# Kernel tuning notes

Measured on AMD Instinct MI355X. Metric: run time of the kernel, lower is better.

The kernel has to match this reference:

```python
import jax, jax.numpy as jnp
import numpy as np

# dims (see shape_source)
B, S, V, E, H, L, F = 512, 17, 40002, 1024, 16, 12, 4096
DH = E // H          # per-head dim = hidden_size // num_attention_heads
NREL = 500           # num_relations
NEDGE = 100          # num_edges (edge-label vocab)
BIG = 1000000.0


def _ln(x, g, b, eps):
    m = jnp.mean(x, axis=-1, keepdims=True)
    v = jnp.mean((x - m) ** 2, axis=-1, keepdims=True)
    return (x - m) * jax.lax.rsqrt(v + eps) * g + b


def setup_inputs() -> dict:
    key = jax.random.key(0)
    ks = jax.random.split(key, 24)
    n = lambda k, sh: 0.02 * jax.random.normal(k, sh, jnp.float32)
    inp = {
        # runtime inputs
        'input_ids': jax.random.randint(ks[0], (B, S), 0, V),
        'input_mask': jnp.ones((B, S), jnp.float32),
        'edge_labels': jax.random.randint(ks[1], (S, S), 0, NEDGE),
        'mask_pos': jax.random.randint(ks[2], (B,), 0, S),
        'mask_label': jax.random.randint(ks[3], (B,), 0, V),
        'mask_type': jnp.ones((B, 1), jnp.float32),  # +1 => entity slot masked
        'confidence': jax.random.uniform(ks[4], (B,), jnp.float32),
        # parameters
        'node_emb': n(ks[5], (V, E)),
        'edge_k': n(ks[6], (NEDGE, DH)),
        'edge_v': n(ks[7], (NEDGE, DH)),
        'ln1_g': jnp.ones((E,), jnp.float32), 'ln1_b': jnp.zeros((E,), jnp.float32),
        'Wq': n(ks[8], (L, E, E)), 'bq': jnp.zeros((L, E), jnp.float32),
        'Wk': n(ks[9], (L, E, E)), 'bk': jnp.zeros((L, E), jnp.float32),
        'Wv': n(ks[10], (L, E, E)), 'bv': jnp.zeros((L, E), jnp.float32),
        'Wo': n(ks[11], (L, E, E)), 'bo': jnp.zeros((L, E), jnp.float32),
        'lnA_g': jnp.ones((L, E), jnp.float32), 'lnA_b': jnp.zeros((L, E), jnp.float32),
        'W1': n(ks[12], (L, E, F)), 'b1': jnp.zeros((L, F), jnp.float32),
        'W2': n(ks[13], (L, F, E)), 'b2': jnp.zeros((L, E), jnp.float32),
        'lnF_g': jnp.ones((L, E), jnp.float32), 'lnF_b': jnp.zeros((L, E), jnp.float32),
        'ln2_g': jnp.ones((E,), jnp.float32), 'ln2_b': jnp.zeros((E,), jnp.float32),
        'fc2_bias': jnp.zeros((V,), jnp.float32),
    }
    return inp


def _forward(node_emb, edge_k, edge_v, ln1_g, ln1_b,
             Wq, bq, Wk, bk, Wv, bv, Wo, bo, lnA_g, lnA_b,
             W1, b1, W2, b2, lnF_g, lnF_b, ln2_g, ln2_b, fc2_bias,
             input_mask, mask_type, confidence,
             input_ids, edge_labels, mask_pos, mask_label):
    # embedding + pre-LN (dropout is identity in eval mode)
    x = _ln(node_emb[input_ids], ln1_g, ln1_b, 1e-12)          # [B,S,E]
    em = jnp.sign(edge_labels).astype(x.dtype)[:, :, None]     # [S,S,1]
    ek = edge_k[edge_labels] * em                              # [S,S,DH]
    ev = edge_v[edge_labels] * em
    m = input_mask[:, :, None]                                 # [B,S,1]
    attn_bias = (BIG * (m @ jnp.swapaxes(m, 1, 2) - 1.0))[:, None]  # [B,1,S,S]

    def step(h, p):
        wq, bq_, wk, bk_, wv, bv_, wo, bo_, ga, ba, w1, b1_, w2, b2_, gf, bf = p
        proj = lambda w, b: (h @ w + b).reshape(B, S, H, DH).transpose(0, 2, 1, 3)
        q = proj(wq, bq_) * (DH ** -0.5)
        k = proj(wk, bk_)
        v = proj(wv, bv_)
        # edge-aware attention scores: content + edge-key bias
        s = jnp.einsum('bhqd,bhkd->bhqk', q, k) \
            + jnp.einsum('bhqd,qkd->bhqk', q, ek) + attn_bias
        a = jax.nn.softmax(s, axis=-1)
        c = jnp.einsum('bhqk,bhkd->bhqd', a, v) \
            + jnp.einsum('bhqk,qkd->bhqd', a, ev)
        y = c.transpose(0, 2, 1, 3).reshape(B, S, E) @ wo + bo_
        h = _ln(h + y, ga, ba, 1e-12)                          # post-LN (cmd 'dan')
        f = jax.nn.gelu(h @ w1 + b1_, approximate=False) @ w2 + b2_
        return _ln(h + f, gf, bf, 1e-12), None

    enc, _ = jax.lax.scan(step, x, (Wq, bq, Wk, bk, Wv, bv, Wo, bo,
                                    lnA_g, lnA_b, W1, b1, W2, b2, lnF_g, lnF_b))

    # mode == 'normal': gather masked position (fc1 output is dead code in the original)
    hm = enc[jnp.arange(B), mask_pos]                          # [B,E]
    hm = _ln(jax.nn.gelu(hm, approximate=False), ln2_g, ln2_b, 1e-7)
    logits = hm @ node_emb.T + fc2_bias                        # tied projection [B,V]

    ti = jnp.concatenate([-jnp.ones((B, NREL), logits.dtype),
                          jnp.ones((B, V - NREL - 2), logits.dtype)], axis=1) * mask_type
    ti = jnp.concatenate([-jnp.ones((B, 2), logits.dtype), ti], axis=1)
    ti = jax.nn.relu(ti)                                       # candidate indicator [B,V]
    logits = logits + BIG * (ti - 1.0)

    oh = jax.nn.one_hot(mask_label, V, dtype=logits.dtype)
    ti2 = ti - oh
    num_cand = jnp.sum(ti2, axis=1)                            # [B]
    sl = ((1.0 + mask_type) * 0.9 + (1.0 - mask_type) * 0.9) / 2.0  # [B,1]
    soft = sl * oh + (1.0 - sl) * ti2 / num_cand[:, None]
    loss = jnp.mean(-jnp.sum(soft * jax.nn.log_softmax(logits, axis=1), axis=1) * confidence)
    return loss, logits


def reference(input_ids, input_mask, edge_labels, mask_pos, mask_label, mask_type,
              confidence, node_emb, edge_k, edge_v, ln1_g, ln1_b, Wq, bq, Wk, bk,
              Wv, bv, Wo, bo, lnA_g, lnA_b, W1, b1, W2, b2, lnF_g, lnF_b,
              ln2_g, ln2_b, fc2_bias):
    return _forward(node_emb, edge_k, edge_v, ln1_g, ln1_b, Wq, bq, Wk, bk, Wv, bv,
                    Wo, bo, lnA_g, lnA_b, W1, b1, W2, b2, lnF_g, lnF_b, ln2_g, ln2_b,
                    fc2_bias, input_mask, mask_type, confidence,
                    input_ids, edge_labels, mask_pos, mask_label)
```

## Files before the change

kernel.cpp:

```cpp
#include <hip/hip_runtime.h>
#include <hip/hip_bf16.h>

#define BB 512
#define SS 17
#define VV 40002
#define VPAD 40064
#define EE 1024
#define HH 16
#define LL 12
#define FF 4096
#define DHD 64
#define NRELC 500
#define MTOK (BB*SS)
#define BIGC 1000000.0f

typedef __bf16 bf16_t;
typedef __bf16 bf16x8 __attribute__((ext_vector_type(8)));
typedef __bf16 bf16x4 __attribute__((ext_vector_type(4)));
typedef float  f32x4  __attribute__((ext_vector_type(4)));

#define GLOAD_LDS16(g, l) __builtin_amdgcn_global_load_lds( \
    (const __attribute__((address_space(1))) void*)(g), \
    (__attribute__((address_space(3))) void*)(l), 16, 0, 0)

__device__ __forceinline__ float dgelu(float x) {
    return 0.5f * x * (1.f + erff(x * 0.70710678118654752f));
}
__device__ __forceinline__ float fgelu(float x) {
    float y = 0.7978845608f * (x + 0.044715f * x * x * x);
    float u = __expf(2.f * y);
    float t = 1.f - 2.f / (u + 1.f);
    return 0.5f * x * (1.f + t);
}

__device__ __forceinline__ float blk_sum(float v, float* sred) {
#pragma unroll
    for (int o = 32; o > 0; o >>= 1) v += __shfl_down(v, o);
    int lane = threadIdx.x & 63, w = threadIdx.x >> 6;
    __syncthreads();
    if (lane == 0) sred[w] = v;
    __syncthreads();
    return sred[0] + sred[1] + sred[2] + sred[3];
}
__device__ __forceinline__ float blk_max(float v, float* sred) {
#pragma unroll
    for (int o = 32; o > 0; o >>= 1) v = fmaxf(v, __shfl_down(v, o));
    int lane = threadIdx.x & 63, w = threadIdx.x >> 6;
    __syncthreads();
    if (lane == 0) sred[w] = v;
    __syncthreads();
    return fmaxf(fmaxf(sred[0], sred[1]), fmaxf(sred[2], sred[3]));
}

__global__ __launch_bounds__(256)
void edge_kernel(const int* __restrict__ labels, const float* __restrict__ eks,
                 const float* __restrict__ evs, float* __restrict__ ek,
                 float* __restrict__ ev) {
    int e = blockIdx.x * 256 + threadIdx.x;
    if (e >= SS * SS * DHD) return;
    int qk = e >> 6, d = e & 63;
    int lab = labels[qk];
    float sgn = lab > 0 ? 1.f : (lab < 0 ? -1.f : 0.f);
    ek[e] = eks[(size_t)lab * DHD + d] * sgn;
    ev[e] = evs[(size_t)lab * DHD + d] * sgn;
}

__global__ __launch_bounds__(256)
void embed_kernel(const int* __restrict__ ids, const float* __restrict__ emb,
                  const float* __restrict__ g, const float* __restrict__ bt,
                  bf16_t* __restrict__ out) {
    __shared__ float sred[4];
    int row = blockIdx.x;
    const float* src = emb + (size_t)ids[row] * EE;
    int c = threadIdx.x * 4;
    float4 x = *(const float4*)(src + c);
    float mean = blk_sum(x.x + x.y + x.z + x.w, sred) * (1.f / EE);
    float x0 = x.x - mean, x1 = x.y - mean, x2 = x.z - mean, x3 = x.w - mean;
    float var = blk_sum(x0*x0 + x1*x1 + x2*x2 + x3*x3, sred) * (1.f / EE);
    float rs = rsqrtf(var + 1e-12f);
    float4 gv = *(const float4*)(g + c), bv = *(const float4*)(bt + c);
    bf16x4 o;
    o[0] = (bf16_t)(x0*rs*gv.x + bv.x); o[1] = (bf16_t)(x1*rs*gv.y + bv.y);
    o[2] = (bf16_t)(x2*rs*gv.z + bv.z); o[3] = (bf16_t)(x3*rs*gv.w + bv.w);
    *(bf16x4*)(out + (size_t)row * EE + c) = o;
}

__global__ __launch_bounds__(256)
void resln_kernel(bf16_t* __restrict__ h, const bf16_t* __restrict__ y,
                  const float* __restrict__ g, const float* __restrict__ bt) {
    __shared__ float sred[4];
    int row = blockIdx.x; int c = threadIdx.x * 4;
    size_t off = (size_t)row * EE + c;
    bf16x4 a = *(const bf16x4*)(h + off), b4 = *(const bf16x4*)(y + off);
    float x0 = (float)a[0] + (float)b4[0], x1 = (float)a[1] + (float)b4[1];
    float x2 = (float)a[2] + (float)b4[2], x3 = (float)a[3] + (float)b4[3];
    float mean = blk_sum(x0 + x1 + x2 + x3, sred) * (1.f / EE);
    x0 -= mean; x1 -= mean; x2 -= mean; x3 -= mean;
    float var = blk_sum(x0*x0 + x1*x1 + x2*x2 + x3*x3, sred) * (1.f / EE);
    float rs = rsqrtf(var + 1e-12f);
    float4 gv = *(const float4*)(g + c), bv = *(const float4*)(bt + c);
    bf16x4 o;
    o[0] = (bf16_t)(x0*rs*gv.x + bv.x); o[1] = (bf16_t)(x1*rs*gv.y + bv.y);
    o[2] = (bf16_t)(x2*rs*gv.z + bv.z); o[3] = (bf16_t)(x3*rs*gv.w + bv.w);
    *(bf16x4*)(h + off) = o;
}

__global__ __launch_bounds__(256)
void hm_kernel(const bf16_t* __restrict__ h, const int* __restrict__ pos,
               const float* __restrict__ g, const float* __restrict__ bt,
               bf16_t* __restrict__ out) {
    __shared__ float sred[4];
    int b = blockIdx.x; int c = threadIdx.x * 4;
    const bf16_t* src = h + ((size_t)(b * SS + pos[b])) * EE + c;
    bf16x4 x = *(const bf16x4*)src;
    float x0 = dgelu((float)x[0]), x1 = dgelu((float)x[1]);
    float x2 = dgelu((float)x[2]), x3 = dgelu((float)x[3]);
    float mean = blk_sum(x0 + x1 + x2 + x3, sred) * (1.f / EE);
    x0 -= mean; x1 -= mean; x2 -= mean; x3 -= mean;
    float var = blk_sum(x0*x0 + x1*x1 + x2*x2 + x3*x3, sred) * (1.f / EE);
    float rs = rsqrtf(var + 1e-7f);
    float4 gv = *(const float4*)(g + c), bv = *(const float4*)(bt + c);
    bf16x4 o;
    o[0] = (bf16_t)(x0*rs*gv.x + bv.x); o[1] = (bf16_t)(x1*rs*gv.y + bv.y);
    o[2] = (bf16_t)(x2*rs*gv.z + bv.z); o[3] = (bf16_t)(x3*rs*gv.w + bv.w);
    *(bf16x4*)(out + (size_t)b * EE + c) = o;
}

__global__ __launch_bounds__(256)
void nodeconv_kernel(const float* __restrict__ src, bf16_t* __restrict__ dst) {
    const size_t total = (size_t)VPAD * (EE / 8);
    for (size_t idx = (size_t)blockIdx.x * 256 + threadIdx.x; idx < total;
         idx += (size_t)gridDim.x * 256) {
        size_t row = idx >> 7;
        bf16x8 o;
#pragma unroll
        for (int u = 0; u < 8; ++u) o[u] = (bf16_t)0.f;
        if (row < VV) {
            const float* s = src + (idx << 3);
            float4 a = *(const float4*)s, b = *(const float4*)(s + 4);
            o[0] = (bf16_t)a.x; o[1] = (bf16_t)a.y; o[2] = (bf16_t)a.z; o[3] = (bf16_t)a.w;
            o[4] = (bf16_t)b.x; o[5] = (bf16_t)b.y; o[6] = (bf16_t)b.z; o[7] = (bf16_t)b.w;
        }
        *(bf16x8*)(dst + (idx << 3)) = o;
    }
}

__global__ __launch_bounds__(256)
void transpose_kernel(const float* __restrict__ Wq, const float* __restrict__ Wk,
                      const float* __restrict__ Wv, const float* __restrict__ Wo,
                      const float* __restrict__ W1, const float* __restrict__ W2,
                      bf16_t* __restrict__ wt) {
    int t = blockIdx.x;
    const float* src; bf16_t* dst; int K, N, tile;
    if (t < 4096) {
        int mi = t >> 10; tile = t & 1023;
        src = mi == 0 ? Wq : mi == 1 ? Wk : mi == 2 ? Wv : Wo;
        dst = wt + (size_t)mi * (1u << 20);
        K = 1024; N = 1024;
    } else if (t < 8192) {
        tile = t - 4096; src = W1; dst = wt + (size_t)4 * (1u << 20); K = 1024; N = 4096;
    } else {
        tile = t - 8192; src = W2; dst = wt + (size_t)8 * (1u << 20); K = 4096; N = 1024;
    }
    int ntiles = N >> 5;
    int kt = tile / ntiles, nt = tile % ntiles;
    __shared__ float lds[32][33];
    int tx = threadIdx.x & 31, ty = threadIdx.x >> 5;
#pragma unroll
    for (int i = 0; i < 4; ++i) {
        int r = ty + i * 8;
        lds[r][tx] = src[(size_t)(kt * 32 + r) * N + nt * 32 + tx];
    }
    __syncthreads();
#pragma unroll
    for (int i = 0; i < 4; ++i) {
        int r = ty + i * 8;
        dst[(size_t)(nt * 32 + r) * K + kt * 32 + tx] = (bf16_t)lds[tx][r];
    }
}

__device__ __forceinline__ void stage_half(const bf16_t* __restrict__ gbase,
                                           bf16_t* sbase, int dstoff, int h,
                                           int t, int K, int srow, int ch, int wid) {
    const bf16_t* s0 = gbase + (size_t)(h * 128 + srow) * K + (size_t)t * 64 + ch * 8;
    const bf16_t* s1 = gbase + (size_t)(h * 128 + 64 + srow) * K + (size_t)t * 64 + ch * 8;
    GLOAD_LDS16(s0, sbase + dstoff + h * 8192 + wid * 512);
    GLOAD_LDS16(s1, sbase + dstoff + h * 8192 + 4096 + wid * 512);
}

template<bool LAST>
__device__ __forceinline__ void ktile256(
    int kt, const bf16_t* __restrict__ Atile, const bf16_t* __restrict__ Btile,
    bf16_t* sA, bf16_t* sB, int K, int srow, int ch, int wid,
    const int (&offA)[8][2], const int (&offB)[4][2], f32x4 (&acc)[8][4]) {
    const int bufo = (kt & 1) << 14;
    const int nbufo = bufo ^ (1 << 14);
    bf16x8 af[4][2], bf0[2][2], bf1[2][2];
    asm volatile("s_waitcnt vmcnt(4)" ::: "memory");
    __builtin_amdgcn_s_barrier();
#pragma unroll
    for (int i = 0; i < 4; ++i)
#pragma unroll
        for (int kk = 0; kk < 2; ++kk)
            af[i][kk] = *(const bf16x8*)(sA + bufo + offA[i][kk]);
#pragma unroll
    for (int j = 0; j < 2; ++j)
#pragma unroll
        for (int kk = 0; kk < 2; ++kk)
            bf0[j][kk] = *(const bf16x8*)(sB + bufo + offB[j][kk]);
    if (!LAST) {
        stage_half(Atile, sA, nbufo, 0, kt + 1, K, srow, ch, wid);
        stage_half(Btile, sB, nbufo, 0, kt + 1, K, srow, ch, wid);
    }
    __builtin_amdgcn_s_setprio(1);
#pragma unroll
    for (int i = 0; i < 4; ++i)
#pragma unroll
        for (int j = 0; j < 2; ++j)
#pragma unroll
            for (int kk = 0; kk < 2; ++kk)
                acc[i][j] = __builtin_amdgcn_mfma_f32_16x16x32_bf16(af[i][kk], bf0[j][kk], acc[i][j], 0, 0, 0);
    __builtin_amdgcn_s_setprio(0);
    if (LAST) asm volatile("s_waitcnt vmcnt(2)" ::: "memory");
    else      asm volatile("s_waitcnt vmcnt(6)" ::: "memory");
    __builtin_amdgcn_s_barrier();
#pragma unroll
    for (int j = 0; j < 2; ++j)
#pragma unroll
        for (int kk = 0; kk < 2; ++kk)
            bf1[j][kk] = *(const bf16x8*)(sB + bufo + offB[2 + j][kk]);
    if (!LAST) stage_half(Btile, sB, nbufo, 1, kt + 1, K, srow, ch, wid);
    __builtin_amdgcn_s_setprio(1);
#pragma unroll
    for (int i = 0; i < 4; ++i)
#pragma unroll
        for (int j = 0; j < 2; ++j)
#pragma unroll
            for (int kk = 0; kk < 2; ++kk)
                acc[i][2 + j] = __builtin_amdgcn_mfma_f32_16x16x32_bf16(af[i][kk], bf1[j][kk], acc[i][2 + j], 0, 0, 0);
    __builtin_amdgcn_s_setprio(0);
    if (LAST) asm volatile("s_waitcnt vmcnt(0)" ::: "memory");
    else      asm volatile("s_waitcnt vmcnt(6)" ::: "memory");
    __builtin_amdgcn_s_barrier();
#pragma unroll
    for (int i = 0; i < 4; ++i)
#pragma unroll
        for (int kk = 0; kk < 2; ++kk)
            af[i][kk] = *(const bf16x8*)(sA + bufo + offA[4 + i][kk]);
    if (!LAST) stage_half(Atile, sA, nbufo, 1, kt + 1, K, srow, ch, wid);
    __builtin_amdgcn_s_setprio(1);
#pragma unroll
    for (int i = 0; i < 4; ++i)
#pragma unroll
        for (int j = 0; j < 2; ++j)
#pragma unroll
            for (int kk = 0; kk < 2; ++kk)
                acc[4 + i][2 + j] = __builtin_amdgcn_mfma_f32_16x16x32_bf16(af[i][kk], bf1[j][kk], acc[4 + i][2 + j], 0, 0, 0);
#pragma unroll
    for (int i = 0; i < 4; ++i)
#pragma unroll
        for (int j = 0; j < 2; ++j)
#pragma unroll
            for (int kk = 0; kk < 2; ++kk)
                acc[4 + i][j] = __builtin_amdgcn_mfma_f32_16x16x32_bf16(af[i][kk], bf0[j][kk], acc[4 + i][j], 0, 0, 0);
    __builtin_amdgcn_s_setprio(0);
}

template<int EPI>
__global__ __launch_bounds__(512, 1)
void gemm256(const bf16_t* __restrict__ A, const bf16_t* __restrict__ B,
             const float* __restrict__ b0, const float* __restrict__ b1,
             const float* __restrict__ b2, bf16_t* __restrict__ C,
             int N, int K) {
    __shared__ __align__(16) bf16_t sA[32768];
    __shared__ __align__(16) bf16_t sB[32768];
    const int tid = threadIdx.x;
    const int lane = tid & 63, wid = tid >> 6;
    const int wm = wid >> 2, wn = wid & 3;
    const int r16 = lane & 15, kblk = lane >> 4;

    const int nwg = gridDim.x * gridDim.y;
    const int wg = blockIdx.y * gridDim.x + blockIdx.x;
    const int q8 = nwg >> 3, r8 = nwg & 7;
    const int xcd = wg & 7, loc = wg >> 3;
    const int swz = (xcd < r8 ? xcd * (q8 + 1) : r8 * (q8 + 1) + (xcd - r8) * q8) + loc;
    const int bm = swz / gridDim.x, bn = swz % gridDim.x;

    f32x4 acc[8][4];
#pragma unroll
    for (int i = 0; i < 8; ++i)
#pragma unroll
        for (int j = 0; j < 4; ++j) acc[i][j] = (f32x4){0.f, 0.f, 0.f, 0.f};

    const bf16_t* Atile = A + (size_t)bm * 256 * K;
    const bf16_t* Btile = B + (size_t)bn * 256 * K;

    const int c = wid * 64 + lane;
    const int srow = c >> 3;
    const int ch = (c & 7) ^ (srow & 7);

    int offA[8][2], offB[4][2];
#pragma unroll
    for (int i = 0; i < 8; ++i) {
        int r = wm * 128 + i * 16 + r16;
#pragma unroll
        for (int kk = 0; kk < 2; ++kk)
            offA[i][kk] = r * 64 + (((kk * 4 + kblk) ^ (r & 7)) << 3);
    }
#pragma unroll
    for (int j = 0; j < 4; ++j) {
        int r = wn * 64 + j * 16 + r16;
#pragma unroll
        for (int kk = 0; kk < 2; ++kk)
            offB[j][kk] = r * 64 + (((kk * 4 + kblk) ^ (r & 7)) << 3);
    }

    stage_half(Atile, sA, 0, 0, 0, K, srow, ch, wid);
    stage_half(Btile, sB, 0, 0, 0, K, srow, ch, wid);
    stage_half(Btile, sB, 0, 1, 0, K, srow, ch, wid);
    stage_half(Atile, sA, 0, 1, 0, K, srow, ch, wid);

    const int nt = K >> 6;
    for (int kt = 0; kt < nt - 1; ++kt)
        ktile256<false>(kt, Atile, Btile, sA, sB, K, srow, ch, wid, offA, offB, acc);
    ktile256<true>(nt - 1, Atile, Btile, sA, sB, K, srow, ch, wid, offA, offB, acc);

    const int crow0 = bm * 256 + wm * 128;
    const int ccol0 = bn * 256 + wn * 64;
#pragma unroll
    for (int i = 0; i < 8; ++i) {
#pragma unroll
        for (int j = 0; j < 4; ++j) {
            int col = ccol0 + j * 16 + r16;
            float bias, scale = 1.f;
            if (EPI == 4) {
                int seg = col >> 10;
                const float* bp = seg == 0 ? b0 : (seg == 1 ? b1 : b2);
                bias = bp[col & 1023];
                if (seg == 0) scale = 0.125f;
            } else {
                bias = b0[col];
            }
#pragma unroll
            for (int r = 0; r < 4; ++r) {
                int rowg = crow0 + i * 16 + kblk * 4 + r;
                float val = acc[i][j][r] + bias;
                if (EPI == 4) val *= scale;
                if (EPI == 2) val = fgelu(val);
                C[(size_t)rowg * N + col] = (bf16_t)val;
            }
        }
    }
}

template<int EPI, bool NB>
__global__ __launch_bounds__(256)
void gemm_bf16(const bf16_t* __restrict__ A, const bf16_t* __restrict__ B,
               const float* __restrict__ b0, const float* __restrict__ mt,
               void* __restrict__ Cout, int M, int N, int K) {
    __shared__ __align__(16) bf16_t sA[3 * 4096];
    __shared__ __align__(16) bf16_t sB[3 * 4096];
    const int tid = threadIdx.x;
    const int lane = tid & 63, wid = tid >> 6;
    const int wm = wid >> 1, wn = wid & 1;
    const int row16 = lane & 15, kblk = lane >> 4;

    const int nwg = gridDim.x * gridDim.y;
    const int wg = blockIdx.y * gridDim.x + blockIdx.x;
    const int q8 = nwg >> 3, r8 = nwg & 7;
    const int xcd = wg & 7, loc = wg >> 3;
    const int swz = (xcd < r8 ? xcd * (q8 + 1) : r8 * (q8 + 1) + (xcd - r8) * q8) + loc;
    const int bm = swz / gridDim.x, bn = swz % gridDim.x;

    f32x4 acc[4][4];
#pragma unroll
    for (int i = 0; i < 4; ++i)
#pragma unroll
        for (int j = 0; j < 4; ++j) acc[i][j] = (f32x4){0.f, 0.f, 0.f, 0.f};

    const bf16_t* Atile = A + (size_t)bm * 128 * K;
    const bf16_t* Btile = B + (size_t)bn * 128 * K;

    const int row_s0 = tid >> 2, chs = tid & 3;
    const int ch0 = chs ^ ((row_s0 >> 1) & 3);
    const int row_s1 = row_s0 + 64;
    const int ch1 = chs ^ ((row_s1 >> 1) & 3);
    const size_t soff0 = (size_t)row_s0 * K + ch0 * 8;
    const size_t soff1 = (size_t)row_s1 * K + ch1 * 8;
    const int ldo0 = wid * 512;
    const int ldo1 = 2048 + wid * 512;

    int offA[4], offB[4];
#pragma unroll
    for (int i = 0; i < 4; ++i) {
        int r = wm * 64 + i * 16 + row16;
        offA[i] = r * 32 + ((kblk ^ ((r >> 1) & 3)) << 3);
    }
#pragma unroll
    for (int j = 0; j < 4; ++j) {
        int r = wn * 64 + j * 16 + row16;
        offB[j] = r * 32 + ((kblk ^ ((r >> 1) & 3)) << 3);
    }

#define STAGE_T(t_, buf_) do { \
        const bf16_t* a_ = Atile + (size_t)(t_) * 32; \
        const bf16_t* b_ = Btile + (size_t)(t_) * 32; \
        bf16_t* dA = sA + (buf_) * 4096; \
        bf16_t* dB = sB + (buf_) * 4096; \
        GLOAD_LDS16(a_ + soff0, dA + ldo0); \
        GLOAD_LDS16(a_ + soff1, dA + ldo1); \
        GLOAD_LDS16(b_ + soff0, dB + ldo0); \
        GLOAD_LDS16(b_ + soff1, dB + ldo1); \
    } while (0)

    const int nt = K >> 5;
    STAGE_T(0, 0);
    STAGE_T(1, 1);
    asm volatile("s_waitcnt vmcnt(4)" ::: "memory");
    __builtin_amdgcn_s_barrier();

    int cur = 0, stg = 2;
    for (int t = 0; t < nt; ++t) {
        const bool more = (t + 2 < nt);
        if (more) {
            STAGE_T(t + 2, stg);
            stg = (stg == 2) ? 0 : stg + 1;
        }
        const bf16_t* bufA = sA + cur * 4096;
        const bf16_t* bufB = sB + cur * 4096;
        bf16x8 af[4], bfr[4];
#pragma unroll
        for (int i = 0; i < 4; ++i) af[i] = *(const bf16x8*)(bufA + offA[i]);
#pragma unroll
        for (int j = 0; j < 4; ++j) bfr[j] = *(const bf16x8*)(bufB + offB[j]);
#pragma unroll
        for (int i = 0; i < 4; ++i)
#pragma unroll
            for (int j = 0; j < 4; ++j)
                acc[i][j] = __builtin_amdgcn_mfma_f32_16x16x32_bf16(af[i], bfr[j], acc[i][j], 0, 0, 0);
        if (t + 1 < nt) {
            if (more) asm volatile("s_waitcnt vmcnt(4)" ::: "memory");
            else      asm volatile("s_waitcnt vmcnt(0)" ::: "memory");
            __builtin_amdgcn_s_barrier();
        }
        cur = (cur == 2) ? 0 : cur + 1;
    }
#undef STAGE_T

    const int crow0 = bm * 128 + wm * 64;
    const int ccol0 = bn * 128 + wn * 64;
#pragma unroll
    for (int i = 0; i < 4; ++i) {
#pragma unroll
        for (int j = 0; j < 4; ++j) {
            int col = ccol0 + j * 16 + row16;
            if (NB && col >= N) continue;
            float bias = b0[col];
#pragma unroll
            for (int r = 0; r < 4; ++r) {
                int rowg = crow0 + i * 16 + kblk * 4 + r;
                float val = acc[i][j][r] + bias;
                if (EPI == 3) {
                    float mtb = mt[rowg];
                    float tt = (col < 2) ? 0.f : fmaxf(0.f, ((col - 2) < NRELC) ? -mtb : mtb);
                    val += BIGC * (tt - 1.f);
                    ((float*)Cout)[(size_t)rowg * N + col] = val;
                } else {
                    ((bf16_t*)Cout)[(size_t)rowg * N + col] = (bf16_t)val;
                }
            }
        }
    }
}

__global__ __launch_bounds__(256)
void attn_kernel(const bf16_t* __restrict__ qkv, const float* __restrict__ ekb,
                 const float* __restrict__ evb, const float* __restrict__ mask,
                 bf16_t* __restrict__ ctx) {
    int bh = blockIdx.x; int b = bh >> 4; int h = bh & 15;
    __shared__ float sq[SS][DHD], sk[SS][DHD], sv[SS][DHD];
    __shared__ float ss[SS][SS + 1];
    __shared__ float sm[SS];
    int tid = threadIdx.x;
    for (int idx = tid; idx < 3 * SS * 8; idx += 256) {
        int t3 = idx / (SS * 8), rc = idx % (SS * 8), s = rc >> 3, c8 = rc & 7;
        bf16x8 v = *(const bf16x8*)(qkv + ((size_t)(b * SS + s)) * 3072 + t3 * 1024 + h * 64 + c8 * 8);
        float* dst = (t3 == 0 ? &sq[0][0] : t3 == 1 ? &sk[0][0] : &sv[0][0]) + s * 64 + c8 * 8;
#pragma unroll
        for (int u = 0; u < 8; ++u) dst[u] = (float)v[u];
    }
    if (tid < SS) sm[tid] = mask[b * SS + tid];
    __syncthreads();
    for (int e = tid; e < SS * SS; e += 256) {
        int qi = e / SS, ki = e % SS;
        const float* ek_ = ekb + (size_t)e * DHD;
        float acc = 0.f;
#pragma unroll 16
        for (int d = 0; d < DHD; ++d) acc += sq[qi][d] * (sk[ki][d] + ek_[d]);
        acc += BIGC * (sm[qi] * sm[ki] - 1.f);
        ss[qi][ki] = acc;
    }
    __syncthreads();
    if (tid < SS) {
        float mx = -1e30f;
        for (int ki = 0; ki < SS; ++ki) mx = fmaxf(mx, ss[tid][ki]);
        float sum = 0.f;
        for (int ki = 0; ki < SS; ++ki) { float e_ = expf(ss[tid][ki] - mx); sum += e_; ss[tid][ki] = e_; }
        float inv = 1.f / sum;
        for (int ki = 0; ki < SS; ++ki) ss[tid][ki] *= inv;
    }
    __syncthreads();
    for (int e = tid; e < SS * DHD; e += 256) {
        int qi = e >> 6, d = e & 63;
        float acc = 0.f;
#pragma unroll
        for (int ki = 0; ki < SS; ++ki)
            acc += ss[qi][ki] * (sv[ki][d] + evb[((size_t)(qi * SS + ki)) * DHD + d]);
        ctx[((size_t)(b * SS + qi)) * EE + h * DHD + d] = (bf16_t)acc;
    }
}

__global__ __launch_bounds__(256)
void loss_part_kernel(const float* __restrict__ logits, const float* __restrict__ mt,
                      const int* __restrict__ label, const float* __restrict__ conf,
                      float* __restrict__ lp) {
    __shared__ float sred[4];
    int b = blockIdx.x;
    const float* row = logits + (size_t)b * VV;
    float mx = -1e30f;
    for (int j = threadIdx.x; j < VV; j += 256) mx = fmaxf(mx, row[j]);
    mx = blk_max(mx, sred);
    float m = mt[b];
    float se = 0.f, s1 = 0.f, cnt = 0.f;
    for (int j = threadIdx.x; j < VV; j += 256) {
        float x = row[j];
        se += expf(x - mx);
        float t = (j < 2) ? 0.f : fmaxf(0.f, ((j - 2) < NRELC) ? -m : m);
        s1 += t * x;
        cnt += t;
    }
    se = blk_sum(se, sred);
    s1 = blk_sum(s1, sred);
    cnt = blk_sum(cnt, sred);
    if (threadIdx.x == 0) {
        float lse = mx + logf(se);
        float lsml = row[label[b]] - lse;
        float num_cand = cnt - 1.f;
        float v = 0.9f * lsml + 0.1f * ((s1 - cnt * lse) - lsml) / num_cand;
        lp[b] = -v * conf[b];
    }
}

__global__ __launch_bounds__(256)
void loss_reduce_kernel(const float* __restrict__ lp, float* __restrict__ out) {
    __shared__ float sred[4];
    float s = 0.f;
    for (int i = threadIdx.x; i < BB; i += 256) s += lp[i];
    s = blk_sum(s, sred);
    if (threadIdx.x == 0) out[0] = s * (1.f / BB);
}

extern "C" void kernel_launch(void* const* d_in, const int* in_sizes, int n_in,
                              void* d_out, int out_size, void* d_ws, size_t ws_size,
                              hipStream_t stream) {
    const int*   input_ids  = (const int*)d_in[0];
    const float* input_mask = (const float*)d_in[1];
    const int*   edge_lab   = (const int*)d_in[2];
    const int*   mask_pos   = (const int*)d_in[3];
    const int*   mask_label = (const int*)d_in[4];
    const float* mask_type  = (const float*)d_in[5];
    const float* confidence = (const float*)d_in[6];
    const float* node_emb   = (const float*)d_in[7];
    const float* edge_k     = (const float*)d_in[8];
    const float* edge_v     = (const float*)d_in[9];
    const float* ln1_g      = (const float*)d_in[10];
    const float* ln1_b      = (const float*)d_in[11];
    const float* Wq         = (const float*)d_in[12];
    const float* bq         = (const float*)d_in[13];
    const float* Wk         = (const float*)d_in[14];
    const float* bk         = (const float*)d_in[15];
    const float* Wv         = (const float*)d_in[16];
    const float* bv         = (const float*)d_in[17];
    const float* Wo         = (const float*)d_in[18];
    const float* bo         = (const float*)d_in[19];
    const float* lnA_g      = (const float*)d_in[20];
    const float* lnA_b      = (const float*)d_in[21];
    const float* W1         = (const float*)d_in[22];
    const float* b1         = (const float*)d_in[23];
    const float* W2         = (const float*)d_in[24];
    const float* b2         = (const float*)d_in[25];
    const float* lnF_g      = (const float*)d_in[26];
    const float* lnF_b      = (const float*)d_in[27];
    const float* ln2_g      = (const float*)d_in[28];
    const float* ln2_b      = (const float*)d_in[29];
    const float* fc2_bias   = (const float*)d_in[30];

    char* p = (char*)d_ws;
    bf16_t* wt    = (bf16_t*)p;
    size_t off = 25165824;
    bf16_t* hbuf  = (bf16_t*)(p + off); off += (size_t)MTOK * EE * 2;
    bf16_t* qkvb  = (bf16_t*)(p + off); off += (size_t)MTOK * FF * 2;
    bf16_t* cb    = (bf16_t*)(p + off); off += (size_t)MTOK * EE * 2;
    bf16_t* yb    = (bf16_t*)(p + off); off += (size_t)MTOK * EE * 2;
    float*  ekb   = (float*)(p + off);  off += (size_t)SS * SS * DHD * 4;
    float*  evb   = (float*)(p + off);  off += (size_t)SS * SS * DHD * 4;
    bf16_t* hmb   = (bf16_t*)(p + off); off += (size_t)BB * EE * 2;
    float*  lp    = (float*)(p + off);  off += (size_t)BB * 4;
    bf16_t* midb  = qkvb;
    bf16_t* nodeb = qkvb;

    float* loss_out   = (float*)d_out;
    float* logits_out = ((float*)d_out) + 1;

    edge_kernel<<<(SS * SS * DHD + 255) / 256, 256, 0, stream>>>(edge_lab, edge_k, edge_v, ekb, evb);
    embed_kernel<<<MTOK, 256, 0, stream>>>(input_ids, node_emb, ln1_g, ln1_b, hbuf);

    dim3 gqkv(3 * EE / 256, MTOK / 256);
    dim3 gffn1(FF / 256, MTOK / 256);
    dim3 gproj(EE / 128, MTOK / 128);

    for (int l = 0; l < LL; ++l) {
        size_t we = (size_t)l * EE * EE;
        size_t wf = (size_t)l * EE * FF;
        transpose_kernel<<<12288, 256, 0, stream>>>(Wq + we, Wk + we, Wv + we, Wo + we,
                                                    W1 + wf, W2 + wf, wt);
        gemm256<4><<<gqkv, 512, 0, stream>>>(hbuf, wt,
            bq + (size_t)l * EE, bk + (size_t)l * EE, bv + (size_t)l * EE,
            qkvb, 3 * EE, EE);
        attn_kernel<<<BB * HH, 256, 0, stream>>>(qkvb, ekb, evb, input_mask, cb);
        gemm_bf16<0, false><<<gproj, 256, 0, stream>>>(cb, wt + (size_t)3 * (1u << 20),
            bo + (size_t)l * EE, nullptr, yb, MTOK, EE, EE);
        resln_kernel<<<MTOK, 256, 0, stream>>>(hbuf, yb, lnA_g + (size_t)l * EE, lnA_b + (size_t)l * EE);
        gemm256<2><<<gffn1, 512, 0, stream>>>(hbuf, wt + (size_t)4 * (1u << 20),
            b1 + (size_t)l * FF, nullptr, nullptr, midb, FF, EE);
        gemm_bf16<0, false><<<gproj, 256, 0, stream>>>(midb, wt + (size_t)8 * (1u << 20),
            b2 + (size_t)l * EE, nullptr, yb, MTOK, EE, FF);
        resln_kernel<<<MTOK, 256, 0, stream>>>(hbuf, yb, lnF_g + (size_t)l * EE, lnF_b + (size_t)l * EE);
    }

    nodeconv_kernel<<<2048, 256, 0, stream>>>(node_emb, nodeb);
    hm_kernel<<<BB, 256, 0, stream>>>(hbuf, mask_pos, ln2_g, ln2_b, hmb);

    dim3 glog(VPAD / 128, BB / 128);
    gemm_bf16<3, true><<<glog, 256, 0, stream>>>(hmb, nodeb, fc2_bias,
        mask_type, logits_out, BB, VV, EE);

    loss_part_kernel<<<BB, 256, 0, stream>>>(logits_out, mask_type, mask_label, confidence, lp);
    loss_reduce_kernel<<<1, 256, 0, stream>>>(lp, loss_out);
}
```

Measured before the change: 5.471 ms.

## Restructure 256x256 GEMM into quadrant-based staging with interleaved per-quadrant MFMA phases

Changes the warp-to-output mapping so each warp owns four 64x32-style quadrants spread across the 256x256 tile rather than one contiguous 128x64 block. The K-tile is staged in four quarter units (A/B halves) that are issued between MFMA phases, with a barrier at the end of each tile in place of the one at the start. The goal is to overlap global-to-LDS loads more evenly with compute and to change the LDS read pattern per phase. In exchange it loads more A fragments per tile (af0 and af1 both live), which raises register pressure, and the wait counts are retuned.

```diff
diff --git a/kernel.cpp b/kernel.cpp
--- a/kernel.cpp
+++ b/kernel.cpp
@@ -179,91 +179,93 @@
     }
 }
 
-__device__ __forceinline__ void stage_half(const bf16_t* __restrict__ gbase,
-                                           bf16_t* sbase, int dstoff, int h,
-                                           int t, int K, int srow, int ch, int wid) {
-    const bf16_t* s0 = gbase + (size_t)(h * 128 + srow) * K + (size_t)t * 64 + ch * 8;
-    const bf16_t* s1 = gbase + (size_t)(h * 128 + 64 + srow) * K + (size_t)t * 64 + ch * 8;
-    GLOAD_LDS16(s0, sbase + dstoff + h * 8192 + wid * 512);
-    GLOAD_LDS16(s1, sbase + dstoff + h * 8192 + 4096 + wid * 512);
+__device__ __forceinline__ void stage_unit256(const bf16_t* __restrict__ op,
+        bf16_t* sOp, int buf, int h, int t, int K,
+        int row0, int ch0, int row1, int ch1, int wid) {
+    const bf16_t* s0 = op + (size_t)(h * 128 + row0) * K + (size_t)t * 64 + ch0 * 8;
+    const bf16_t* s1 = op + (size_t)(h * 128 + row1) * K + (size_t)t * 64 + ch1 * 8;
+    bf16_t* d = sOp + buf * 16384 + h * 8192 + wid * 1024;
+    GLOAD_LDS16(s0, d);
+    GLOAD_LDS16(s1, d + 512);
 }
 
 template<bool LAST>
 __device__ __forceinline__ void ktile256(
-    int kt, const bf16_t* __restrict__ Atile, const bf16_t* __restrict__ Btile,
-    bf16_t* sA, bf16_t* sB, int K, int srow, int ch, int wid,
-    const int (&offA)[8][2], const int (&offB)[4][2], f32x4 (&acc)[8][4]) {
-    const int bufo = (kt & 1) << 14;
-    const int nbufo = bufo ^ (1 << 14);
-    bf16x8 af[4][2], bf0[2][2], bf1[2][2];
-    asm volatile("s_waitcnt vmcnt(4)" ::: "memory");
-    __builtin_amdgcn_s_barrier();
+    int t, const bf16_t* __restrict__ Atile, const bf16_t* __restrict__ Btile,
+    bf16_t* sA, bf16_t* sB, int K,
+    int row0, int ch0, int row1, int ch1, int wid,
+    const int (&offA)[4][2], const int (&offB)[2][2], f32x4 (&acc)[8][4]) {
+    const int cur = (t & 1) * 16384;
+    const int nxt = cur ^ 16384;
+    bf16x8 af0[4][2], af1[4][2], bf0[2][2], bf1[2][2];
 #pragma unroll
     for (int i = 0; i < 4; ++i)
 #pragma unroll
         for (int kk = 0; kk < 2; ++kk)
-            af[i][kk] = *(const bf16x8*)(sA + bufo + offA[i][kk]);
-#pragma unroll
-    for (int j = 0; j < 2; ++j)
+            af0[i][kk] = *(const bf16x8*)(sA + cur + offA[i][kk]);
+#pragma unroll
+    for (int jj = 0; jj < 2; ++jj)
 #pragma unroll
         for (int kk = 0; kk < 2; ++kk)
-            bf0[j][kk] = *(const bf16x8*)(sB + bufo + offB[j][kk]);
-    if (!LAST) {
-        stage_half(Atile, sA, nbufo, 0, kt + 1, K, srow, ch, wid);
-        stage_half(Btile, sB, nbufo, 0, kt + 1, K, srow, ch, wid);
-    }
+            bf0[jj][kk] = *(const bf16x8*)(sB + cur + offB[jj][kk]);
+    if (!LAST) stage_unit256(Atile, sA, 1 - (t & 1), 0, t + 1, K, row0, ch0, row1, ch1, wid);
     __builtin_amdgcn_s_setprio(1);
 #pragma unroll
     for (int i = 0; i < 4; ++i)
 #pragma unroll
-        for (int j = 0; j < 2; ++j)
+        for (int jj = 0; jj < 2; ++jj)
 #pragma unroll
             for (int kk = 0; kk < 2; ++kk)
-                acc[i][j] = __builtin_amdgcn_mfma_f32_16x16x32_bf16(af[i][kk], bf0[j][kk], acc[i][j], 0, 0, 0);
+                acc[i][jj] = __builtin_amdgcn_mfma_f32_16x16x32_bf16(af0[i][kk], bf0[jj][kk], acc[i][jj], 0, 0, 0);
     __builtin_amdgcn_s_setprio(0);
     if (LAST) asm volatile("s_waitcnt vmcnt(2)" ::: "memory");
-    else      asm volatile("s_waitcnt vmcnt(6)" ::: "memory");
+    else      asm volatile("s_waitcnt vmcnt(4)" ::: "memory");
     __builtin_amdgcn_s_barrier();
 #pragma unroll
-    for (int j = 0; j < 2; ++j)
+    for (int i = 0; i < 4; ++i)
 #pragma unroll
         for (int kk = 0; kk < 2; ++kk)
-            bf1[j][kk] = *(const bf16x8*)(sB + bufo + offB[2 + j][kk]);
-    if (!LAST) stage_half(Btile, sB, nbufo, 1, kt + 1, K, srow, ch, wid);
+            af1[i][kk] = *(const bf16x8*)(sA + cur + 8192 + offA[i][kk]);
+    if (!LAST) stage_unit256(Btile, sB, 1 - (t & 1), 0, t + 1, K, row0, ch0, row1, ch1, wid);
     __builtin_amdgcn_s_setprio(1);
 #pragma unroll
     for (int i = 0; i < 4; ++i)
 #pragma unroll
-        for (int j = 0; j < 2; ++j)
+        for (int jj = 0; jj < 2; ++jj)
 #pragma unroll
             for (int kk = 0; kk < 2; ++kk)
-                acc[i][2 + j] = __builtin_amdgcn_mfma_f32_16x16x32_bf16(af[i][kk], bf1[j][kk], acc[i][2 + j], 0, 0, 0);
+                acc[4 + i][jj] = __builtin_amdgcn_mfma_f32_16x16x32_bf16(af1[i][kk], bf0[jj][kk], acc[4 + i][jj], 0, 0, 0);
     __builtin_amdgcn_s_setprio(0);
     if (LAST) asm volatile("s_waitcnt vmcnt(0)" ::: "memory");
-    else      asm volatile("s_waitcnt vmcnt(6)" ::: "memory");
+    else      asm volatile("s_waitcnt vmcnt(4)" ::: "memory");
     __builtin_amdgcn_s_barrier();
 #pragma unroll
+    for (int jj = 0; jj < 2; ++jj)
+#pragma unroll
+        for (int kk = 0; kk < 2; ++kk)
+            bf1[jj][kk] = *(const bf16x8*)(sB + cur + 8192 + offB[jj][kk]);
+    if (!LAST) stage_unit256(Atile, sA, 1 - (t & 1), 1, t + 1, K, row0, ch0, row1, ch1, wid);
+    __builtin_amdgcn_s_setprio(1);
+#pragma unroll
     for (int i = 0; i < 4; ++i)
 #pragma unroll
-        for (int kk = 0; kk < 2; ++kk)
-            af[i][kk] = *(const bf16x8*)(sA + bufo + offA[4 + i][kk]);
-    if (!LAST) stage_half(Atile, sA, nbufo, 1, kt + 1, K, srow, ch, wid);
-    __builtin_amdgcn_s_setprio(1);
+        for (int jj = 0; jj < 2; ++jj)
+#pragma unroll
+            for (int kk = 0; kk < 2; ++kk)
+                acc[4 + i][2 + jj] = __builtin_amdgcn_mfma_f32_16x16x32_bf16(af1[i][kk], bf1[jj][kk], acc[4 + i][2 + jj], 0, 0, 0);
+    if (!LAST) stage_unit256(Btile, sB, 1 - (t & 1), 1, t + 1, K, row0, ch0, row1, ch1, wid);
 #pragma unroll
     for (int i = 0; i < 4; ++i)
 #pragma unroll
-        for (int j = 0; j < 2; ++j)
+        for (int jj = 0; jj < 2; ++jj)
 #pragma unroll
             for (int kk = 0; kk < 2; ++kk)
-                acc[4 + i][2 + j] = __builtin_amdgcn_mfma_f32_16x16x32_bf16(af[i][kk], bf1[j][kk], acc[4 + i][2 + j], 0, 0, 0);
-#pragma unroll
-    for (int i = 0; i < 4; ++i)
-#pragma unroll
-        for (int j = 0; j < 2; ++j)
-#pragma unroll
-            for (int kk = 0; kk < 2; ++kk)
-                acc[4 + i][j] = __builtin_amdgcn_mfma_f32_16x16x32_bf16(af[i][kk], bf0[j][kk], acc[4 + i][j], 0, 0, 0);
+                acc[i][2 + jj] = __builtin_amdgcn_mfma_f32_16x16x32_bf16(af0[i][kk], bf1[jj][kk], acc[i][2 + jj], 0, 0, 0);
     __builtin_amdgcn_s_setprio(0);
+    if (!LAST) {
+        asm volatile("s_waitcnt vmcnt(4)" ::: "memory");
+        __builtin_amdgcn_s_barrier();
+    }
 }
 
 template<int EPI>
@@ -295,43 +297,48 @@
     const bf16_t* Atile = A + (size_t)bm * 256 * K;
     const bf16_t* Btile = B + (size_t)bn * 256 * K;
 
-    const int c = wid * 64 + lane;
-    const int srow = c >> 3;
-    const int ch = (c & 7) ^ (srow & 7);
-
-    int offA[8][2], offB[4][2];
-#pragma unroll
-    for (int i = 0; i < 8; ++i) {
-        int r = wm * 128 + i * 16 + r16;
+    const int row0 = wid * 16 + (lane >> 3);
+    const int row1 = row0 + 8;
+    const int ch0 = (lane & 7) ^ (row0 & 7);
+    const int ch1 = (lane & 7) ^ (row1 & 7);
+
+    int offA[4][2], offB[2][2];
+#pragma unroll
+    for (int i = 0; i < 4; ++i) {
+        int r = wm * 64 + i * 16 + r16;
 #pragma unroll
         for (int kk = 0; kk < 2; ++kk)
             offA[i][kk] = r * 64 + (((kk * 4 + kblk) ^ (r & 7)) << 3);
     }
 #pragma unroll
-    for (int j = 0; j < 4; ++j) {
-        int r = wn * 64 + j * 16 + r16;
+    for (int jj = 0; jj < 2; ++jj) {
+        int r = wn * 32 + jj * 16 + r16;
 #pragma unroll
         for (int kk = 0; kk < 2; ++kk)
-            offB[j][kk] = r * 64 + (((kk * 4 + kblk) ^ (r & 7)) << 3);
-    }
-
-    stage_half(Atile, sA, 0, 0, 0, K, srow, ch, wid);
-    stage_half(Btile, sB, 0, 0, 0, K, srow, ch, wid);
-    stage_half(Btile, sB, 0, 1, 0, K, srow, ch, wid);
-    stage_half(Atile, sA, 0, 1, 0, K, srow, ch, wid);
+            offB[jj][kk] = r * 64 + (((kk * 4 + kblk) ^ (r & 7)) << 3);
+    }
+
+    stage_unit256(Atile, sA, 0, 0, 0, K, row0, ch0, row1, ch1, wid);
+    stage_unit256(Btile, sB, 0, 0, 0, K, row0, ch0, row1, ch1, wid);
+    stage_unit256(Atile, sA, 0, 1, 0, K, row0, ch0, row1, ch1, wid);
+    stage_unit256(Btile, sB, 0, 1, 0, K, row0, ch0, row1, ch1, wid);
+    asm volatile("s_waitcnt vmcnt(4)" ::: "memory");
+    __builtin_amdgcn_s_barrier();
 
     const int nt = K >> 6;
-    for (int kt = 0; kt < nt - 1; ++kt)
-        ktile256<false>(kt, Atile, Btile, sA, sB, K, srow, ch, wid, offA, offB, acc);
-    ktile256<true>(nt - 1, Atile, Btile, sA, sB, K, srow, ch, wid, offA, offB, acc);
-
-    const int crow0 = bm * 256 + wm * 128;
-    const int ccol0 = bn * 256 + wn * 64;
-#pragma unroll
-    for (int i = 0; i < 8; ++i) {
-#pragma unroll
-        for (int j = 0; j < 4; ++j) {
-            int col = ccol0 + j * 16 + r16;
+    for (int t = 0; t < nt - 1; ++t)
+        ktile256<false>(t, Atile, Btile, sA, sB, K, row0, ch0, row1, ch1, wid, offA, offB, acc);
+    ktile256<true>(nt - 1, Atile, Btile, sA, sB, K, row0, ch0, row1, ch1, wid, offA, offB, acc);
+
+#pragma unroll
+    for (int qi = 0; qi < 2; ++qi)
+#pragma unroll
+    for (int i = 0; i < 4; ++i) {
+#pragma unroll
+        for (int qj = 0; qj < 2; ++qj)
+#pragma unroll
+        for (int jj = 0; jj < 2; ++jj) {
+            int col = bn * 256 + qj * 128 + wn * 32 + jj * 16 + r16;
             float bias, scale = 1.f;
             if (EPI == 4) {
                 int seg = col >> 10;
@@ -343,8 +350,8 @@
             }
 #pragma unroll
             for (int r = 0; r < 4; ++r) {
-                int rowg = crow0 + i * 16 + kblk * 4 + r;
-                float val = acc[i][j][r] + bias;
+                int rowg = bm * 256 + qi * 128 + wm * 64 + i * 16 + kblk * 4 + r;
+                float val = acc[qi * 4 + i][qj * 2 + jj][r] + bias;
                 if (EPI == 4) val *= scale;
                 if (EPI == 2) val = fgelu(val);
                 C[(size_t)rowg * N + col] = (bf16_t)val;
```

After: 5.777 ms. 5.6% more time.
